# Kernel optimization log

Hardware: AMD Instinct MI355X
Metric: run time of the kernel (lower is better)

## Reference

```python
import jax, jax.numpy as jnp
import numpy as np

NUM_LAYERS, NUM_HEADS, DH, C = 5, 4, 32, 128
B, T, HH, WW = 2, 12, 32, 32


def conv2d(x, w, b):
    # x: (N, Cin, H, W), w: (Cout, Cin, 3, 3) same padding
    y = jax.lax.conv_general_dilated(x, w, window_strides=(1, 1), padding='SAME',
                                     dimension_numbers=('NCHW', 'OIHW', 'NCHW'))
    return y + b[None, :, None, None]


def sine_pos(length, depth):
    pos = jnp.arange(length, dtype=jnp.float32)[:, None]
    div = jnp.exp(jnp.arange(0, depth, 2, dtype=jnp.float32) * (-np.log(10000.0) / depth))
    pe = jnp.zeros((length, depth), dtype=jnp.float32)
    pe = pe.at[:, 0::2].set(jnp.sin(pos * div))
    pe = pe.at[:, 1::2].set(jnp.cos(pos * div))
    return pe[None, :, :, None, None]  # (1, L, dh, 1, 1) broadcasts over batch & spatial


def group_norm(x, scale, bias, groups=4, eps=1e-5):
    n, c, h, w = x.shape
    xg = x.reshape(n, groups, c // groups, h, w)
    mu = xg.mean(axis=(2, 3, 4), keepdims=True)
    var = ((xg - mu) ** 2).mean(axis=(2, 3, 4), keepdims=True)
    xg = (xg - mu) * jax.lax.rsqrt(var + eps)
    return xg.reshape(n, c, h, w) * scale[None, :, None, None] + bias[None, :, None, None]


def head_forward(x, pos, qw, qb, kvw, kvb, aw, ab):
    # x: (B, L, dh, H, W)
    b, l, c, h, w = x.shape
    xf = x.reshape(b * l, c, h, w)
    q = conv2d(xf, qw, qb).reshape(b, l, c, h, w) + pos
    v = conv2d(xf, kvw, kvb).reshape(b, l, c, h, w)  # k and v share features
    k = v + pos
    # pairwise concat: (B, Lq, Lk, 2*dh, H, W)
    qe = jnp.broadcast_to(q[:, :, None], (b, l, l, c, h, w))
    ke = jnp.broadcast_to(k[:, None, :], (b, l, l, c, h, w))
    qk = jnp.concatenate([qe, ke], axis=3).reshape(b * l * l, 2 * c, h, w)
    att = conv2d(qk, aw, ab).reshape(b, l, l, 1, h, w)
    att = jax.nn.softmax(att, axis=2)  # softmax over key-frame axis
    return jnp.sum(att * v[:, None], axis=2)  # (B, L, dh, H, W)


def reference(input_tensor, q_w, q_b, kv_w, kv_b, att_w, att_b,
              ff1_w, ff1_b, ff2_w, ff2_b, gn_w, gn_b):
    num_layers, num_heads = q_w.shape[0], q_w.shape[1]
    b, l, c, h, w = input_tensor.shape
    dh = c // num_heads
    pos = sine_pos(l, dh)
    out = input_tensor
    for li in range(num_layers):
        heads = [head_forward(out[:, :, i * dh:(i + 1) * dh], pos,
                              q_w[li, i], q_b[li, i], kv_w[li, i], kv_b[li, i],
                              att_w[li, i], att_b[li, i])
                 for i in range(num_heads)]
        att_out = jnp.concatenate(heads, axis=2) + out  # residual
        att_flat = att_out.reshape(b * l, c, h, w)
        ff = conv2d(jax.nn.relu(conv2d(att_flat, ff1_w[li], ff1_b[li])), ff2_w[li], ff2_b[li])
        y = group_norm(ff + att_flat, gn_w[li], gn_b[li])
        out = y.reshape(b, l, c, h, w)
    return out


def setup_inputs() -> dict:
    key = jax.random.key(0)
    ks = jax.random.split(key, 12)
    f = lambda k, s, sc=1.0: jax.random.normal(k, s, dtype=jnp.float32) * sc
    L, H = NUM_LAYERS, NUM_HEADS
    return {
        'input_tensor': f(ks[0], (B, T, C, HH, WW)),
        'q_w': f(ks[1], (L, H, DH, DH, 3, 3), 0.05),
        'q_b': f(ks[2], (L, H, DH), 0.05),
        'kv_w': f(ks[3], (L, H, DH, DH, 3, 3), 0.05),
        'kv_b': f(ks[4], (L, H, DH), 0.05),
        'att_w': f(ks[5], (L, H, 1, 2 * DH, 3, 3), 0.05),
        'att_b': f(ks[6], (L, H, 1), 0.05),
        'ff1_w': f(ks[7], (L, C, C, 3, 3), 0.03),
        'ff1_b': f(ks[8], (L, C), 0.03),
        'ff2_w': f(ks[9], (L, C, C, 3, 3), 0.03),
        'ff2_b': f(ks[10], (L, C), 0.03),
        'gn_w': jnp.ones((L, C), dtype=jnp.float32),
        'gn_b': jnp.zeros((L, C), dtype=jnp.float32),
    }
```

## Files before the change

kernel.cpp:

```cpp
#include <hip/hip_runtime.h>

#define NELEM 3145728
#define IMG 24
#define CH 128
#define HW 1024

using short8   = __attribute__((ext_vector_type(8))) short;
using ushort4v = __attribute__((ext_vector_type(4))) unsigned short;
using float4v  = __attribute__((ext_vector_type(4))) float;
using float16v = __attribute__((ext_vector_type(16))) float;

__device__ inline unsigned short f2bf(float f){
    union { float f; unsigned u; } c; c.f = f;
    return (unsigned short)((c.u + 0x7FFF + ((c.u >> 16) & 1)) >> 16);
}

__global__ __launch_bounds__(256) void k_prep(
    const float* __restrict__ ff1w, const float* __restrict__ ff2w,
    const float* __restrict__ kvw, const float* __restrict__ input,
    unsigned short* __restrict__ Wd, unsigned short* __restrict__ Wkv,
    float* __restrict__ cur)
{
    const int t = threadIdx.x;
    __shared__ float tile[32 * 132];
    if (blockIdx.x < 5760) {
        int idx = blockIdx.x * 256 + t;
        int li2 = idx / 147456, r1 = idx - li2 * 147456;
        int j = r1 & 7, co = (r1 >> 3) & 127;
        int kh = (r1 >> 10) & 1, k16 = (r1 >> 11) & 7, tap = r1 >> 14;
        int ci = k16 * 16 + kh * 8 + j;
        const float* base = ((li2 & 1) ? ff2w : ff1w) + (size_t)(li2 >> 1) * 147456;
        Wd[idx] = f2bf(base[(co * 128 + ci) * 9 + tap]);
    } else if (blockIdx.x < 6480) {
        int idx = (blockIdx.x - 5760) * 256 + t;
        int li = idx / 36864, r1 = idx - li * 36864;
        int j = r1 & 7, co = (r1 >> 3) & 127;
        int kh = (r1 >> 10) & 1, k16 = (r1 >> 11) & 1, tap = r1 >> 12;
        int h = co >> 5, colc = co & 31, cil = k16 * 16 + kh * 8 + j;
        Wkv[idx] = f2bf(kvw[((size_t)((li * 4 + h) * 32 + colc) * 32 + cil) * 9 + tap]);
    } else {
        int bb = blockIdx.x - 6480;
        int img = bb >> 5, px0 = (bb & 31) * 32;
        #pragma unroll
        for (int it = 0; it < 4; it++) {
            int c = it * 32 + (t >> 3), pxq = t & 7;
            float4v val = *(const float4v*)(input + ((size_t)img * 128 + c) * HW + px0 + pxq * 4);
            #pragma unroll
            for (int j = 0; j < 4; j++) tile[(pxq * 4 + j) * 132 + c] = val[j];
        }
        __syncthreads();
        #pragma unroll
        for (int it = 0; it < 4; it++) {
            int px = it * 8 + (t >> 5), cq = t & 31;
            float4v o = *(float4v*)(tile + px * 132 + cq * 4);
            *(float4v*)(cur + ((size_t)img * HW + px0 + px) * 128 + cq * 4) = o;
        }
    }
}

__global__ __launch_bounds__(256, 2) void k_kvattn(
    const float* __restrict__ cur, const unsigned short* __restrict__ wkv,
    const float* __restrict__ kvb, const float* __restrict__ aw,
    const float* __restrict__ pstatp, const float* __restrict__ gw,
    const float* __restrict__ gb, float* __restrict__ v,
    float* __restrict__ ak, float* __restrict__ pstatz)
{
    const int img = blockIdx.x, h = blockIdx.y, y0 = blockIdx.z * 8;
    const int t = threadIdx.x;
    const int b = img / 12, l = img - b * 12;

    if (blockIdx.x == 0 && blockIdx.y == 0 && blockIdx.z == 0 && t < 192)
        pstatz[t] = 0.f;

    __shared__ float sxv[32 * 341];
    __shared__ unsigned short slab[408 * 40];
    __shared__ float spos[32], sbias[32], sgw[32], sgb[32];

    if (t < 32) {
        int j2 = t & ~1;
        float freq = __expf(-(float)j2 * 0.28782313662425576f);
        float ang = (float)l * freq;
        spos[t] = (t & 1) ? __cosf(ang) : __sinf(ang);
        sbias[t] = kvb[h * 32 + t];
        sgw[t] = gw ? gw[h * 32 + t] : 1.f;
        sgb[t] = gb ? gb[h * 32 + t] : 0.f;
    }
    float mu = 0.f, inv = 1.f;
    if (pstatp) {
        float S = pstatp[(img * 4 + h) * 2], Q = pstatp[(img * 4 + h) * 2 + 1];
        mu = S * (1.f / 32768.f);
        inv = rsqrtf(Q * (1.f / 32768.f) - mu * mu + 1e-5f);
    }
    __syncthreads();

    for (int u = t; u < 3264; u += 256) {
        int q = u & 7, p = u >> 3;
        int lr = p / 34, lc = p - lr * 34;
        int yr = y0 - 2 + lr, x = lc - 1;
        float4v val = (float4v){0.f, 0.f, 0.f, 0.f};
        if (yr >= 0 && yr < 32 && x >= 0 && x < 32) {
            val = *(const float4v*)(cur + ((size_t)img * HW + yr * 32 + x) * 128 + h * 32 + q * 4);
            #pragma unroll
            for (int j = 0; j < 4; j++)
                val[j] = (val[j] - mu) * inv * sgw[q * 4 + j] + sgb[q * 4 + j];
        }
        ushort4v o;
        #pragma unroll
        for (int j = 0; j < 4; j++) o[j] = f2bf(val[j]);
        *(ushort4v*)(slab + p * 40 + q * 4) = o;
    }
    __syncthreads();

    const int lane = t & 63, wave = t >> 6;
    const int colx = lane & 31, kh = lane >> 5;
    const short8* w8 = reinterpret_cast<const short8*>(wkv);

    for (int f = wave; f < 10; f += 4) {
        float16v acc;
        #pragma unroll
        for (int r = 0; r < 16; r++) acc[r] = 0.f;
        #pragma unroll
        for (int tap = 0; tap < 9; tap++) {
            const int ky = tap / 3, kx = tap - ky * 3;
            #pragma unroll
            for (int k16 = 0; k16 < 2; k16++) {
                short8 a = *reinterpret_cast<const short8*>(
                    slab + ((f + ky) * 34 + colx + kx) * 40 + k16 * 16 + kh * 8);
                short8 bf = w8[((tap * 2 + k16) * 2 + kh) * 128 + h * 32 + colx];
                acc = __builtin_amdgcn_mfma_f32_32x32x16_bf16(a, bf, acc, 0, 0, 0);
            }
        }
        const int yr = y0 - 1 + f;
        const bool rowin = (yr >= 0 && yr < 32);
        const bool vown = rowin && f >= 1 && f <= 8;
        const float posci = spos[colx], bb = sbias[colx];
        float* vrow = v + ((size_t)img * HW + yr * 32) * 128 + h * 32 + colx;
        #pragma unroll
        for (int r = 0; r < 16; r++) {
            int x2 = (r & 3) + 8 * (r >> 2) + 4 * kh;
            float val = rowin ? acc[r] + bb : 0.f;
            if (vown) vrow[(size_t)x2 * 128] = val;
            sxv[colx * 341 + f * 34 + x2 + 1] = rowin ? val + posci : 0.f;
        }
    }
    for (int u = t; u < 640; u += 256) {
        int ci = u & 31, r2 = u >> 5;
        sxv[ci * 341 + (r2 >> 1) * 34 + ((r2 & 1) ? 33 : 0)] = 0.f;
    }
    __syncthreads();

    const float* wb = aw + (h * 64 + 32) * 9;
    const int r = t >> 5, xx = t & 31;
    float acc2 = 0.f;
    #pragma unroll 4
    for (int ci = 0; ci < 32; ci++) {
        #pragma unroll
        for (int ky = 0; ky < 3; ky++)
            #pragma unroll
            for (int kx = 0; kx < 3; kx++)
                acc2 = fmaf(sxv[ci * 341 + (r + ky) * 34 + xx + kx],
                            wb[ci * 9 + ky * 3 + kx], acc2);
    }
    ak[((size_t)(b * 4 + h) * 12 + l) * HW + (y0 + r) * 32 + xx] = acc2;
}

__global__ __launch_bounds__(256, 2) void k_ffn(
    const float* __restrict__ cin, const unsigned short* __restrict__ w1,
    const float* __restrict__ b1, const unsigned short* __restrict__ w2,
    const float* __restrict__ b2, float* __restrict__ cout,
    float* __restrict__ pstat)
{
    const int img = blockIdx.x, y = blockIdx.y;
    const int t = threadIdx.x;
    const int wave = t >> 6, lane = t & 63;
    const int colx = lane & 31, kh = lane >> 5;
    const int cog = wave * 32;

    __shared__ __align__(16) char smem[46240];
    unsigned short* s1 = (unsigned short*)smem;
    unsigned short* s2 = (unsigned short*)smem;
    float* sOut = (float*)(smem + 28288);

    for (int u = t; u < 5440; u += 256) {
        int q = u & 31, p = u >> 5;
        int lr = p / 34, lc = p - lr * 34;
        int yr = y - 2 + lr, x = lc - 1;
        float4v val = (float4v){0.f, 0.f, 0.f, 0.f};
        if (yr >= 0 && yr < 32 && x >= 0 && x < 32)
            val = *(const float4v*)(cin + ((size_t)img * HW + yr * 32 + x) * 128 + q * 4);
        ushort4v o;
        #pragma unroll
        for (int j = 0; j < 4; j++) o[j] = f2bf(val[j]);
        *(ushort4v*)(s1 + p * 136 + q * 4) = o;
    }

    const short8* w8a = reinterpret_cast<const short8*>(w1);
    const short8* w8b = reinterpret_cast<const short8*>(w2);
    const int bl = kh * 128 + cog + colx;

    float16v acc[3];
    #pragma unroll
    for (int f = 0; f < 3; f++)
        #pragma unroll
        for (int r = 0; r < 16; r++) acc[f][r] = 0.f;

    short8 B9[9];
    #pragma unroll
    for (int tap = 0; tap < 9; tap++)
        B9[tap] = w8a[(tap * 8 + 0) * 256 + bl];

    __syncthreads();

    #pragma unroll
    for (int k16 = 0; k16 < 8; k16++) {
        if (k16) {
            #pragma unroll
            for (int tap = 0; tap < 9; tap++)
                B9[tap] = w8a[(tap * 8 + k16) * 256 + bl];
        }
        #pragma unroll
        for (int ar = 0; ar < 5; ar++) {
            #pragma unroll
            for (int kx = 0; kx < 3; kx++) {
                short8 a = *reinterpret_cast<const short8*>(
                    s1 + (ar * 34 + kx + colx) * 136 + kh * 8 + k16 * 16);
                #pragma unroll
                for (int ky = 0; ky < 3; ky++) {
                    const int f = ar - ky;
                    if (f >= 0 && f < 3)
                        acc[f] = __builtin_amdgcn_mfma_f32_32x32x16_bf16(
                            a, B9[ky * 3 + kx], acc[f], 0, 0, 0);
                }
            }
        }
    }

    short8 bfr[8];
    auto loadB2 = [&](int tap){
        #pragma unroll
        for (int k16 = 0; k16 < 8; k16++)
            bfr[k16] = w8b[(tap * 8 + k16) * 256 + bl];
    };
    loadB2(0);
    __syncthreads();

    {
        const int co = cog + colx;
        const float bb1 = b1[co];
        #pragma unroll
        for (int f = 0; f < 3; f++) {
            const bool rowin = (y - 1 + f >= 0) && (y - 1 + f < 32);
            #pragma unroll
            for (int r = 0; r < 16; r++) {
                int x2 = (r & 3) + 8 * (r >> 2) + 4 * kh;
                float val = rowin ? fmaxf(acc[f][r] + bb1, 0.f) : 0.f;
                s2[(f * 34 + x2 + 1) * 136 + co] = f2bf(val);
            }
        }
    }
    for (int u = t; u < 768; u += 256) {
        int c = u & 127, rr = u >> 7;
        s2[((rr >> 1) * 34 + ((rr & 1) ? 33 : 0)) * 136 + c] = 0;
    }
    __syncthreads();

    float16v a2;
    #pragma unroll
    for (int r = 0; r < 16; r++) a2[r] = 0.f;
    #pragma unroll
    for (int tap = 0; tap < 9; tap++) {
        if (tap) loadB2(tap);
        const int ky = tap / 3, kx = tap - ky * 3;
        #pragma unroll
        for (int k16 = 0; k16 < 8; k16++) {
            short8 a = *reinterpret_cast<const short8*>(
                s2 + (ky * 34 + kx + colx) * 136 + kh * 8 + k16 * 16);
            a2 = __builtin_amdgcn_mfma_f32_32x32x16_bf16(a, bfr[k16], a2, 0, 0, 0);
        }
    }
    __syncthreads();

    {
        const int co = cog + colx;
        const float bb2 = b2[co];
        #pragma unroll
        for (int r = 0; r < 16; r++) {
            int x2 = (r & 3) + 8 * (r >> 2) + 4 * kh;
            sOut[x2 * 132 + co] = a2[r] + bb2;
        }
    }
    __syncthreads();

    float ps1 = 0.f, ps2 = 0.f;
    #pragma unroll
    for (int it = 0; it < 4; it++) {
        int u = it * 256 + t;
        int px = u >> 5, cq = u & 31;
        size_t gi = ((size_t)img * HW + y * 32 + px) * 128 + cq * 4;
        float4v rv = *(const float4v*)(cin + gi);
        float4v ov;
        #pragma unroll
        for (int j = 0; j < 4; j++) {
            ov[j] = sOut[px * 132 + cq * 4 + j] + rv[j];
            ps1 += ov[j]; ps2 += ov[j] * ov[j];
        }
        *(float4v*)(cout + gi) = ov;
    }
    ps1 += __shfl_xor(ps1, 1);  ps2 += __shfl_xor(ps2, 1);
    ps1 += __shfl_xor(ps1, 2);  ps2 += __shfl_xor(ps2, 2);
    ps1 += __shfl_xor(ps1, 4);  ps2 += __shfl_xor(ps2, 4);
    ps1 += __shfl_xor(ps1, 32); ps2 += __shfl_xor(ps2, 32);
    if ((lane & 39) == 0) {
        int g = (lane & 31) >> 3;
        atomicAdd(&pstat[(img * 4 + g) * 2], ps1);
        atomicAdd(&pstat[(img * 4 + g) * 2 + 1], ps2);
    }
}

__global__ __launch_bounds__(256) void k_wsum(const float* __restrict__ ak,
    const float* __restrict__ v, float* __restrict__ cur,
    const float* __restrict__ pstatp, const float* __restrict__ gw,
    const float* __restrict__ gb)
{
    int gid = blockIdx.x * 256 + threadIdx.x;
    int c = gid & 127, px = (gid >> 7) & 1023, b = gid >> 17;
    int h = c >> 5;
    const float* wp = ak + ((size_t)(b * 4 + h) * 12) * HW + px;
    float a[12], m = -1e30f;
    #pragma unroll
    for (int l = 0; l < 12; l++) { a[l] = wp[l * HW]; m = fmaxf(m, a[l]); }
    float ssum = 0.f;
    #pragma unroll
    for (int l = 0; l < 12; l++) { a[l] = __expf(a[l] - m); ssum += a[l]; }
    float invs = 1.f / ssum;
    const float* vp = v + ((size_t)(b * 12) * HW + px) * 128 + c;
    float s = 0.f;
    #pragma unroll
    for (int l = 0; l < 12; l++) s += a[l] * vp[(size_t)l * HW * 128];
    s *= invs;
    float gwv = gw ? gw[c] : 1.f, gbv = gb ? gb[c] : 0.f;
    float* cp = cur + ((size_t)(b * 12) * HW + px) * 128 + c;
    #pragma unroll
    for (int l = 0; l < 12; l++) {
        int img = b * 12 + l;
        float mu = 0.f, inv = 1.f;
        if (pstatp) {
            float S = pstatp[(img * 4 + h) * 2], Q = pstatp[(img * 4 + h) * 2 + 1];
            mu = S * (1.f / 32768.f);
            inv = rsqrtf(Q * (1.f / 32768.f) - mu * mu + 1e-5f);
        }
        float cv = cp[(size_t)l * HW * 128];
        cp[(size_t)l * HW * 128] = (cv - mu) * inv * gwv + gbv + s;
    }
}

__global__ __launch_bounds__(256) void k_gnlast(const float* __restrict__ y,
    const float* __restrict__ pstat, const float* __restrict__ gw,
    const float* __restrict__ gb, float* __restrict__ outp)
{
    int gid = blockIdx.x * 256 + threadIdx.x;
    int px4 = (gid & 255) * 4, c = (gid >> 8) & 127, img = gid >> 15;
    int g = c >> 5;
    float S = pstat[(img * 4 + g) * 2], Q = pstat[(img * 4 + g) * 2 + 1];
    float mu = S * (1.f / 32768.f);
    float inv = rsqrtf(Q * (1.f / 32768.f) - mu * mu + 1e-5f);
    float gg = gw[c], bb = gb[c];
    float4v o;
    #pragma unroll
    for (int j = 0; j < 4; j++) {
        float val = y[((size_t)img * HW + px4 + j) * 128 + c];
        o[j] = (val - mu) * inv * gg + bb;
    }
    *(float4v*)(outp + ((size_t)img * 128 + c) * HW + px4) = o;
}

extern "C" void kernel_launch(void* const* d_in, const int* in_sizes, int n_in,
                              void* d_out, int out_size, void* d_ws, size_t ws_size,
                              hipStream_t stream)
{
    const float* input = (const float*)d_in[0];
    const float* kv_w  = (const float*)d_in[3];
    const float* kv_b  = (const float*)d_in[4];
    const float* att_w = (const float*)d_in[5];
    const float* ff1_w = (const float*)d_in[7];
    const float* ff1_b = (const float*)d_in[8];
    const float* ff2_w = (const float*)d_in[9];
    const float* ff2_b = (const float*)d_in[10];
    const float* gn_w  = (const float*)d_in[11];
    const float* gn_b  = (const float*)d_in[12];

    float* ws  = (float*)d_ws;
    float* c0  = ws;
    float* c1  = c0 + (size_t)NELEM;
    float* ak  = c1 + (size_t)NELEM;
    float* pstat = ak + 98304;
    unsigned short* W2d  = (unsigned short*)(pstat + 384);
    unsigned short* W2kv = W2d + 1474560;
    float* v    = (float*)d_out;
    float* outp = (float*)d_out;

    k_prep<<<7248, 256, 0, stream>>>(ff1_w, ff2_w, kv_w, input, W2d, W2kv, c0);

    for (int li = 0; li < 5; li++) {
        float* cin  = (li & 1) ? c1 : c0;
        float* cout = (li & 1) ? c0 : c1;
        float* psC = pstat + (li & 1) * 192;
        const float* psP = li ? pstat + ((li - 1) & 1) * 192 : nullptr;
        const float* gwP = li ? gn_w + (li - 1) * 128 : nullptr;
        const float* gbP = li ? gn_b + (li - 1) * 128 : nullptr;

        k_kvattn<<<dim3(IMG, 4, 4), 256, 0, stream>>>(
            cin, W2kv + (size_t)li * 36864, kv_b + li * 128, att_w + (size_t)li * 2304,
            psP, gwP, gbP, v, ak, psC);
        k_wsum<<<1024, 256, 0, stream>>>(ak, v, cin, psP, gwP, gbP);
        k_ffn<<<dim3(IMG, 32), 256, 0, stream>>>(
            cin, W2d + (size_t)(li * 2 + 0) * 147456, ff1_b + li * 128,
            W2d + (size_t)(li * 2 + 1) * 147456, ff2_b + li * 128, cout, psC);
    }
    k_gnlast<<<3072, 256, 0, stream>>>(c1, pstat + 0, gn_w + 4 * 128,
                                       gn_b + 4 * 128, outp);
}
```

Measured before the change: 439.5 us.

## Process two output rows per FFN block with 512 threads to cut halo recompute

The fused FFN kernel now handles two image rows per block using 8 waves. Each half of the waves computes two of the four intermediate ReLU rows and one output row. This reduces the redundant first-conv halo work (4 intermediate rows per 2 outputs instead of 3 per 1) and halves the number of input halo loads. In exchange shared memory per block grows and the launch bound asks for 4 blocks of 512 threads per CU, which may force register spilling.

```diff
diff --git a/kernel.cpp b/kernel.cpp
--- a/kernel.cpp
+++ b/kernel.cpp
@@ -164,27 +164,28 @@
     ak[((size_t)(b * 4 + h) * 12 + l) * HW + (y0 + r) * 32 + xx] = acc2;
 }
 
-__global__ __launch_bounds__(256, 2) void k_ffn(
+__global__ __launch_bounds__(512, 4) void k_ffn(
     const float* __restrict__ cin, const unsigned short* __restrict__ w1,
     const float* __restrict__ b1, const unsigned short* __restrict__ w2,
     const float* __restrict__ b2, float* __restrict__ cout,
     float* __restrict__ pstat)
 {
-    const int img = blockIdx.x, y = blockIdx.y;
+    const int img = blockIdx.x, y0 = blockIdx.y * 2;
     const int t = threadIdx.x;
     const int wave = t >> 6, lane = t & 63;
     const int colx = lane & 31, kh = lane >> 5;
-    const int cog = wave * 32;
-
-    __shared__ __align__(16) char smem[46240];
+    const int cog = (wave & 3) * 32;
+    const int fh = wave >> 2;
+
+    __shared__ __align__(16) char smem[55488];
     unsigned short* s1 = (unsigned short*)smem;
     unsigned short* s2 = (unsigned short*)smem;
-    float* sOut = (float*)(smem + 28288);
-
-    for (int u = t; u < 5440; u += 256) {
+    float* sOut = (float*)smem;
+
+    for (int u = t; u < 6528; u += 512) {
         int q = u & 31, p = u >> 5;
         int lr = p / 34, lc = p - lr * 34;
-        int yr = y - 2 + lr, x = lc - 1;
+        int yr = y0 - 2 + lr, x = lc - 1;
         float4v val = (float4v){0.f, 0.f, 0.f, 0.f};
         if (yr >= 0 && yr < 32 && x >= 0 && x < 32)
             val = *(const float4v*)(cin + ((size_t)img * HW + yr * 32 + x) * 128 + q * 4);
@@ -198,9 +199,9 @@
     const short8* w8b = reinterpret_cast<const short8*>(w2);
     const int bl = kh * 128 + cog + colx;
 
-    float16v acc[3];
-    #pragma unroll
-    for (int f = 0; f < 3; f++)
+    float16v acc[2];
+    #pragma unroll
+    for (int f = 0; f < 2; f++)
         #pragma unroll
         for (int r = 0; r < 16; r++) acc[f][r] = 0.f;
 
@@ -219,17 +220,18 @@
                 B9[tap] = w8a[(tap * 8 + k16) * 256 + bl];
         }
         #pragma unroll
-        for (int ar = 0; ar < 5; ar++) {
+        for (int ai = 0; ai < 4; ai++) {
+            const int ar = 2 * fh + ai;
             #pragma unroll
             for (int kx = 0; kx < 3; kx++) {
                 short8 a = *reinterpret_cast<const short8*>(
                     s1 + (ar * 34 + kx + colx) * 136 + kh * 8 + k16 * 16);
                 #pragma unroll
                 for (int ky = 0; ky < 3; ky++) {
-                    const int f = ar - ky;
-                    if (f >= 0 && f < 3)
-                        acc[f] = __builtin_amdgcn_mfma_f32_32x32x16_bf16(
-                            a, B9[ky * 3 + kx], acc[f], 0, 0, 0);
+                    const int fi = ai - ky;
+                    if (fi >= 0 && fi < 2)
+                        acc[fi] = __builtin_amdgcn_mfma_f32_32x32x16_bf16(
+                            a, B9[ky * 3 + kx], acc[fi], 0, 0, 0);
                 }
             }
         }
@@ -248,17 +250,19 @@
         const int co = cog + colx;
         const float bb1 = b1[co];
         #pragma unroll
-        for (int f = 0; f < 3; f++) {
-            const bool rowin = (y - 1 + f >= 0) && (y - 1 + f < 32);
+        for (int fi = 0; fi < 2; fi++) {
+            const int f_rel = 2 * fh + fi;
+            const int yr = y0 - 1 + f_rel;
+            const bool rowin = (yr >= 0 && yr < 32);
             #pragma unroll
             for (int r = 0; r < 16; r++) {
                 int x2 = (r & 3) + 8 * (r >> 2) + 4 * kh;
-                float val = rowin ? fmaxf(acc[f][r] + bb1, 0.f) : 0.f;
-                s2[(f * 34 + x2 + 1) * 136 + co] = f2bf(val);
+                float val = rowin ? fmaxf(acc[fi][r] + bb1, 0.f) : 0.f;
+                s2[(f_rel * 34 + x2 + 1) * 136 + co] = f2bf(val);
             }
         }
     }
-    for (int u = t; u < 768; u += 256) {
+    for (int u = t; u < 1024; u += 512) {
         int c = u & 127, rr = u >> 7;
         s2[((rr >> 1) * 34 + ((rr & 1) ? 33 : 0)) * 136 + c] = 0;
     }
@@ -274,7 +278,7 @@
         #pragma unroll
         for (int k16 = 0; k16 < 8; k16++) {
             short8 a = *reinterpret_cast<const short8*>(
-                s2 + (ky * 34 + kx + colx) * 136 + kh * 8 + k16 * 16);
+                s2 + ((fh + ky) * 34 + kx + colx) * 136 + kh * 8 + k16 * 16);
             a2 = __builtin_amdgcn_mfma_f32_32x32x16_bf16(a, bfr[k16], a2, 0, 0, 0);
         }
     }
@@ -286,7 +290,7 @@
         #pragma unroll
         for (int r = 0; r < 16; r++) {
             int x2 = (r & 3) + 8 * (r >> 2) + 4 * kh;
-            sOut[x2 * 132 + co] = a2[r] + bb2;
+            sOut[(fh * 32 + x2) * 132 + co] = a2[r] + bb2;
         }
     }
     __syncthreads();
@@ -294,14 +298,15 @@
     float ps1 = 0.f, ps2 = 0.f;
     #pragma unroll
     for (int it = 0; it < 4; it++) {
-        int u = it * 256 + t;
-        int px = u >> 5, cq = u & 31;
-        size_t gi = ((size_t)img * HW + y * 32 + px) * 128 + cq * 4;
+        int u = it * 512 + t;
+        int pxi = u >> 5, cq = u & 31;
+        int r2 = pxi >> 5, x = pxi & 31;
+        size_t gi = ((size_t)img * HW + (y0 + r2) * 32 + x) * 128 + cq * 4;
         float4v rv = *(const float4v*)(cin + gi);
         float4v ov;
         #pragma unroll
         for (int j = 0; j < 4; j++) {
-            ov[j] = sOut[px * 132 + cq * 4 + j] + rv[j];
+            ov[j] = sOut[(r2 * 32 + x) * 132 + cq * 4 + j] + rv[j];
             ps1 += ov[j]; ps2 += ov[j] * ov[j];
         }
         *(float4v*)(cout + gi) = ov;
@@ -413,7 +418,7 @@
             cin, W2kv + (size_t)li * 36864, kv_b + li * 128, att_w + (size_t)li * 2304,
             psP, gwP, gbP, v, ak, psC);
         k_wsum<<<1024, 256, 0, stream>>>(ak, v, cin, psP, gwP, gbP);
-        k_ffn<<<dim3(IMG, 32), 256, 0, stream>>>(
+        k_ffn<<<dim3(IMG, 16), 512, 0, stream>>>(
             cin, W2d + (size_t)(li * 2 + 0) * 147456, ff1_b + li * 128,
             W2d + (size_t)(li * 2 + 1) * 147456, ff2_b + li * 128, cout, psC);
     }
```

Result: slower. 459.7 us (+4.6%).
